# Kernel optimization log

Measured on AMD Instinct MI355X. Metric: run time of the kernel, lower is better.

The kernel has to match this reference:

```python
import jax, jax.numpy as jnp
import numpy as np
import math

# Hardcoded model constants (from source globals)
N_LAYERS = 4
MAX_SEQ_LEN = 34
VOCAB_SIZE = 14
TOK_DIM = 3
POS_DIM = 3
D_MODEL = 6
HEAD_DIM = 3
N_POS = 10
MAX_DIGITS = 10
ANSWER_LEN = 11
X_START, PLUS_POS, Y_START, EQ_POS, Z_START, EOS_POS = 0, 10, 11, 21, 22, 33
PLUS_TOKEN, EQUALS_TOKEN, EOS_TOKEN, PAD_TOKEN = 10, 11, 12, 13
BATCH = 16384


def _spiral(i, p):
    return (math.cos(2 * math.pi * i / p), math.sin(2 * math.pi * i / p), i / max(p - 1, 1))


def _build_pos_enc():
    pe = np.zeros((MAX_SEQ_LEN, POS_DIM), np.float32)
    for i in range(MAX_DIGITS):
        pe[X_START + i] = _spiral(i, N_POS)
    for i in range(MAX_DIGITS):
        pe[Y_START + i] = _spiral(i, N_POS)
    for i in range(min(ANSWER_LEN, N_POS)):
        pe[Z_START + i] = _spiral(i, N_POS)
    pe[Z_START + 10] = [0.0, 0.0, 1.5]
    pe[PLUS_POS] = [2.0, 0.0, -1.0]
    pe[EQ_POS] = [0.0, 2.0, -1.0]
    pe[EOS_POS] = [-2.0, 0.0, -1.0]
    return jnp.asarray(pe)


def _build_tok_emb():
    emb = np.zeros((VOCAB_SIZE, TOK_DIM), np.float32)
    for d in range(10):
        emb[d] = _spiral(d, 10)
    emb[PLUS_TOKEN] = [2.0, 0.0, -1.0]
    emb[EQUALS_TOKEN] = [0.0, 2.0, -1.0]
    emb[EOS_TOKEN] = [-2.0, 0.0, -1.0]
    emb[PAD_TOKEN] = [0.0, -2.0, -1.0]
    return jnp.asarray(emb)


def _xavier(key, shape):
    fan_out, fan_in = shape[-2], shape[-1]
    bound = math.sqrt(6.0 / (fan_in + fan_out))
    return jax.random.uniform(key, shape, jnp.float32, -bound, bound)


def setup_inputs() -> dict:
    key = jax.random.key(0)
    ks = jax.random.split(key, 10)
    L = N_LAYERS
    return {
        "idx": jax.random.randint(ks[0], (BATCH, MAX_SEQ_LEN), 0, VOCAB_SIZE),
        "tok_emb": _build_tok_emb(),
        "pos_enc": _build_pos_enc(),
        "ln_w": jnp.ones((L, D_MODEL), jnp.float32),
        "ln_b": jnp.zeros((L, D_MODEL), jnp.float32),
        "q1w": _xavier(ks[1], (L, HEAD_DIM, TOK_DIM)),
        "k1w": _xavier(ks[2], (L, HEAD_DIM, TOK_DIM)),
        "v1w": _xavier(ks[3], (L, HEAD_DIM, TOK_DIM)),
        "q2w": _xavier(ks[4], (L, HEAD_DIM, POS_DIM)),
        "k2w": _xavier(ks[5], (L, HEAD_DIM, POS_DIM)),
        "v2w": _xavier(ks[6], (L, HEAD_DIM, POS_DIM)),
        "out_w": _xavier(ks[7], (L, D_MODEL, 2 * HEAD_DIM)),
        "lnf_w": jnp.ones((D_MODEL,), jnp.float32),
        "lnf_b": jnp.zeros((D_MODEL,), jnp.float32),
        "head_w": _xavier(ks[8], (VOCAB_SIZE, D_MODEL)),
    }


def _layernorm(x, w, b, eps=1e-5):
    m = jnp.mean(x, -1, keepdims=True)
    v = jnp.mean(jnp.square(x - m), -1, keepdims=True)
    return (x - m) * jax.lax.rsqrt(v + eps) * w + b


def _attend(q, k, v, mask):
    # q,k,v: [B,T,HEAD_DIM]; mask: [T,T] bool lower-triangular
    s = jnp.einsum('bqd,bkd->bqk', q, k) / math.sqrt(HEAD_DIM)
    s = jnp.where(mask, s, jnp.finfo(s.dtype).min)
    return jnp.einsum('bqk,bkd->bqd', jax.nn.softmax(s, axis=-1), v)


def reference(idx, tok_emb, pos_enc, ln_w, ln_b, q1w, k1w, v1w, q2w, k2w, v2w, out_w, lnf_w, lnf_b, head_w):
    B, T = idx.shape
    tok = tok_emb[idx]                                   # [B,T,3]
    pos = jnp.broadcast_to(pos_enc[:T], (B, T, POS_DIM))  # [B,T,3]
    x = jnp.concatenate([tok, pos], axis=-1)             # [B,T,6]
    mask = jnp.tril(jnp.ones((T, T), bool))
    for l in range(N_LAYERS):
        h = _layernorm(x, ln_w[l], ln_b[l])
        ht, hp = h[..., :TOK_DIM], h[..., TOK_DIM:]
        o1 = _attend(ht @ q1w[l].T, ht @ k1w[l].T, ht @ v1w[l].T, mask)
        o2 = _attend(hp @ q2w[l].T, hp @ k2w[l].T, hp @ v2w[l].T, mask)
        x = x + jnp.concatenate([o1, o2], axis=-1) @ out_w[l].T
    x = _layernorm(x, lnf_w, lnf_b)
    return x @ head_w.T                                  # [B,T,VOCAB]
```

## Files before the change

kernel.cpp:

```cpp
#include <hip/hip_runtime.h>
#include <math.h>

#define N_LAYERS 4
#define SEQ      34
#define BATCH_N  16384
#define NE       16
#define NSLOT    8
#define NT       5
#define VOCAB    14
#define QSCALE   0.8329806647638704f

__global__ __launch_bounds__(128) void addtrans_kernel(
    const int*   __restrict__ idx,
    const float* __restrict__ tok_emb,
    const float* __restrict__ pos_enc,
    const float* __restrict__ ln_w,
    const float* __restrict__ ln_b,
    const float* __restrict__ q1w,
    const float* __restrict__ k1w,
    const float* __restrict__ v1w,
    const float* __restrict__ q2w,
    const float* __restrict__ k2w,
    const float* __restrict__ v2w,
    const float* __restrict__ out_w,
    const float* __restrict__ lnf_w,
    const float* __restrict__ lnf_b,
    const float* __restrict__ head_w,
    float* __restrict__ out)
{
    __shared__ float4 kvs[3 * SEQ + 1][NE];

    const int x = threadIdx.x & (NE - 1);
    const int y = threadIdx.x >> 4;
    const int b = (int)blockIdx.x * NE + x;

    int tp[NT];
    tp[0] = (y < 2) ? (32 + y) : (24 + y);
    tp[1] = y;
    tp[2] = 8 + y;
    tp[3] = 16 + y;
    tp[4] = (y < 2) ? (24 + y) : -1;
    const int jmax = tp[0];

    float xs[NT][6];
    #pragma unroll
    for (int k = 0; k < NT; ++k) {
        const int t = tp[k];
        if (t >= 0) {
            const int tok = idx[(size_t)b * SEQ + t];
            xs[k][0] = tok_emb[tok * 3 + 0];
            xs[k][1] = tok_emb[tok * 3 + 1];
            xs[k][2] = tok_emb[tok * 3 + 2];
            xs[k][3] = pos_enc[t * 3 + 0];
            xs[k][4] = pos_enc[t * 3 + 1];
            xs[k][5] = pos_enc[t * 3 + 2];
        }
    }

    float qs[NT][6];

    for (int l = 0; l < N_LAYERS; ++l) {
        __syncthreads();

        #pragma unroll
        for (int k = 0; k < NT; ++k) {
            const int t = tp[k];
            if (t >= 0) {
                float h[6];
                {
                    const float* v = xs[k];
                    float m = (v[0]+v[1]+v[2]+v[3]+v[4]+v[5]) * (1.0f/6.0f);
                    float var = 0.f;
                    #pragma unroll
                    for (int i = 0; i < 6; ++i) { float d = v[i]-m; var += d*d; }
                    var *= (1.0f/6.0f);
                    float r = rsqrtf(var + 1e-5f);
                    #pragma unroll
                    for (int i = 0; i < 6; ++i)
                        h[i] = (v[i]-m) * r * ln_w[l*6+i] + ln_b[l*6+i];
                }
                float kk[6], vv[6];
                #pragma unroll
                for (int i = 0; i < 3; ++i) {
                    const int w = l*9 + i*3;
                    qs[k][i]   = (q1w[w]*h[0] + q1w[w+1]*h[1] + q1w[w+2]*h[2]) * QSCALE;
                    kk[i]      =  k1w[w]*h[0] + k1w[w+1]*h[1] + k1w[w+2]*h[2];
                    vv[i]      =  v1w[w]*h[0] + v1w[w+1]*h[1] + v1w[w+2]*h[2];
                    qs[k][3+i] = (q2w[w]*h[3] + q2w[w+1]*h[4] + q2w[w+2]*h[5]) * QSCALE;
                    kk[3+i]    =  k2w[w]*h[3] + k2w[w+1]*h[4] + k2w[w+2]*h[5];
                    vv[3+i]    =  v2w[w]*h[3] + v2w[w+1]*h[4] + v2w[w+2]*h[5];
                }
                kvs[0*SEQ + t][x] = make_float4(kk[0], kk[1], kk[2], kk[3]);
                kvs[1*SEQ + t][x] = make_float4(kk[4], kk[5], vv[0], vv[1]);
                kvs[2*SEQ + t][x] = make_float4(vv[2], vv[3], vv[4], vv[5]);
            }
        }
        __syncthreads();

        float l1[NT], l2[NT], a[NT][6];
        #pragma unroll
        for (int k = 0; k < NT; ++k) {
            l1[k] = 0.f; l2[k] = 0.f;
            #pragma unroll
            for (int i = 0; i < 6; ++i) a[k][i] = 0.f;
        }
        float4 c0 = kvs[0][x], c1 = kvs[SEQ][x], c2 = kvs[2*SEQ][x];
        #pragma unroll 2
        for (int j = 0; j <= jmax; ++j) {
            float4 n0 = kvs[j + 1][x];
            float4 n1 = kvs[SEQ + j + 1][x];
            float4 n2 = kvs[2*SEQ + j + 1][x];
            #pragma unroll
            for (int k = 0; k < NT; ++k) {
                if (k == 0 || j <= tp[k]) {
                    float s1 = qs[k][0]*c0.x + qs[k][1]*c0.y + qs[k][2]*c0.z;
                    float s2 = qs[k][3]*c0.w + qs[k][4]*c1.x + qs[k][5]*c1.y;
                    float p1 = __builtin_amdgcn_exp2f(s1);
                    float p2 = __builtin_amdgcn_exp2f(s2);
                    l1[k] += p1;        l2[k] += p2;
                    a[k][0] += p1*c1.z; a[k][1] += p1*c1.w; a[k][2] += p1*c2.x;
                    a[k][3] += p2*c2.y; a[k][4] += p2*c2.z; a[k][5] += p2*c2.w;
                }
            }
            c0 = n0; c1 = n1; c2 = n2;
        }

        #pragma unroll
        for (int k = 0; k < NT; ++k) {
            if (tp[k] >= 0) {
                const float i1 = __builtin_amdgcn_rcpf(l1[k]);
                const float i2 = __builtin_amdgcn_rcpf(l2[k]);
                float o[6] = { a[k][0]*i1, a[k][1]*i1, a[k][2]*i1,
                               a[k][3]*i2, a[k][4]*i2, a[k][5]*i2 };
                #pragma unroll
                for (int i = 0; i < 6; ++i) {
                    const int w = l*36 + i*6;
                    xs[k][i] += out_w[w+0]*o[0] + out_w[w+1]*o[1] + out_w[w+2]*o[2]
                              + out_w[w+3]*o[3] + out_w[w+4]*o[4] + out_w[w+5]*o[5];
                }
            }
        }
    }

    #pragma unroll
    for (int k = 0; k < NT; ++k) {
        const int t = tp[k];
        if (t >= 0) {
            float hf[6];
            {
                const float* v = xs[k];
                float m = (v[0]+v[1]+v[2]+v[3]+v[4]+v[5]) * (1.0f/6.0f);
                float var = 0.f;
                #pragma unroll
                for (int i = 0; i < 6; ++i) { float d = v[i]-m; var += d*d; }
                var *= (1.0f/6.0f);
                float r = rsqrtf(var + 1e-5f);
                #pragma unroll
                for (int i = 0; i < 6; ++i)
                    hf[i] = (v[i]-m) * r * lnf_w[i] + lnf_b[i];
            }
            float lg[VOCAB];
            #pragma unroll
            for (int c = 0; c < VOCAB; ++c) {
                const int w = c*6;
                lg[c] = head_w[w+0]*hf[0] + head_w[w+1]*hf[1] + head_w[w+2]*hf[2]
                      + head_w[w+3]*hf[3] + head_w[w+4]*hf[4] + head_w[w+5]*hf[5];
            }
            float2* op = (float2*)(out + ((size_t)b * SEQ + t) * VOCAB);
            #pragma unroll
            for (int c = 0; c < 7; ++c)
                op[c] = make_float2(lg[2*c], lg[2*c+1]);
        }
    }
}

extern "C" void kernel_launch(void* const* d_in, const int* in_sizes, int n_in,
                              void* d_out, int out_size, void* d_ws, size_t ws_size,
                              hipStream_t stream) {
    const int*   idx     = (const int*)  d_in[0];
    const float* tok_emb = (const float*)d_in[1];
    const float* pos_enc = (const float*)d_in[2];
    const float* ln_w    = (const float*)d_in[3];
    const float* ln_b    = (const float*)d_in[4];
    const float* q1w     = (const float*)d_in[5];
    const float* k1w     = (const float*)d_in[6];
    const float* v1w     = (const float*)d_in[7];
    const float* q2w     = (const float*)d_in[8];
    const float* k2w     = (const float*)d_in[9];
    const float* v2w     = (const float*)d_in[10];
    const float* out_w   = (const float*)d_in[11];
    const float* lnf_w   = (const float*)d_in[12];
    const float* lnf_b   = (const float*)d_in[13];
    const float* head_w  = (const float*)d_in[14];
    float* out = (float*)d_out;

    const int grid = BATCH_N / NE;
    addtrans_kernel<<<grid, NE * NSLOT, 0, stream>>>(
        idx, tok_emb, pos_enc, ln_w, ln_b,
        q1w, k1w, v1w, q2w, k2w, v2w,
        out_w, lnf_w, lnf_b, head_w, out);
}
```

Baseline: 146.2 us.

## Restructure causal attention loop into fully unrolled blocks with static row masks

Reassigns rows so each thread holds positions y, 8+y, 16+y, 24+y (plus 32+y for two slots) and rewrites the key loop as a fully unrolled 4x8 block structure. Rows whose keys are entirely in the past are processed unconditionally, and only the diagonal block needs a per-thread mask. This removes the runtime branch per row per key and the software prefetch rotation. It also adds a launch_bounds occupancy hint of 2 blocks. Full unrolling increases code size and may raise register pressure.

```diff
diff --git a/kernel.cpp b/kernel.cpp
--- a/kernel.cpp
+++ b/kernel.cpp
@@ -6,11 +6,22 @@
 #define BATCH_N  16384
 #define NE       16
 #define NSLOT    8
-#define NT       5
+#define NROW     5
 #define VOCAB    14
 #define QSCALE   0.8329806647638704f
 
-__global__ __launch_bounds__(128) void addtrans_kernel(
+#define ATT_BODY(m)                                                        \
+    {                                                                      \
+        float s1 = qs[m][0]*c0.x + qs[m][1]*c0.y + qs[m][2]*c0.z;          \
+        float s2 = qs[m][3]*c0.w + qs[m][4]*c1.x + qs[m][5]*c1.y;          \
+        float p1 = __builtin_amdgcn_exp2f(s1);                             \
+        float p2 = __builtin_amdgcn_exp2f(s2);                             \
+        l1[m] += p1;          l2[m] += p2;                                 \
+        a[m][0] += p1*c1.z;   a[m][1] += p1*c1.w;   a[m][2] += p1*c2.x;    \
+        a[m][3] += p2*c2.y;   a[m][4] += p2*c2.z;   a[m][5] += p2*c2.w;    \
+    }
+
+__global__ __launch_bounds__(128, 2) void addtrans_kernel(
     const int*   __restrict__ idx,
     const float* __restrict__ tok_emb,
     const float* __restrict__ pos_enc,
@@ -34,17 +45,16 @@
     const int y = threadIdx.x >> 4;
     const int b = (int)blockIdx.x * NE + x;
 
-    int tp[NT];
-    tp[0] = (y < 2) ? (32 + y) : (24 + y);
-    tp[1] = y;
-    tp[2] = 8 + y;
-    tp[3] = 16 + y;
-    tp[4] = (y < 2) ? (24 + y) : -1;
-    const int jmax = tp[0];
-
-    float xs[NT][6];
+    int tp[NROW];
+    tp[0] = y;
+    tp[1] = 8 + y;
+    tp[2] = 16 + y;
+    tp[3] = 24 + y;
+    tp[4] = (y < 2) ? (32 + y) : -1;
+
+    float xs[NROW][6];
     #pragma unroll
-    for (int k = 0; k < NT; ++k) {
+    for (int k = 0; k < NROW; ++k) {
         const int t = tp[k];
         if (t >= 0) {
             const int tok = idx[(size_t)b * SEQ + t];
@@ -57,13 +67,13 @@
         }
     }
 
-    float qs[NT][6];
+    float qs[NROW][6];
 
     for (int l = 0; l < N_LAYERS; ++l) {
         __syncthreads();
 
         #pragma unroll
-        for (int k = 0; k < NT; ++k) {
+        for (int k = 0; k < NROW; ++k) {
             const int t = tp[k];
             if (t >= 0) {
                 float h[6];
@@ -97,53 +107,55 @@
         }
         __syncthreads();
 
-        float l1[NT], l2[NT], a[NT][6];
-        #pragma unroll
-        for (int k = 0; k < NT; ++k) {
+        float l1[NROW], l2[NROW], a[NROW][6];
+        #pragma unroll
+        for (int k = 0; k < NROW; ++k) {
             l1[k] = 0.f; l2[k] = 0.f;
             #pragma unroll
             for (int i = 0; i < 6; ++i) a[k][i] = 0.f;
         }
-        float4 c0 = kvs[0][x], c1 = kvs[SEQ][x], c2 = kvs[2*SEQ][x];
-        #pragma unroll 2
-        for (int j = 0; j <= jmax; ++j) {
-            float4 n0 = kvs[j + 1][x];
-            float4 n1 = kvs[SEQ + j + 1][x];
-            float4 n2 = kvs[2*SEQ + j + 1][x];
-            #pragma unroll
-            for (int k = 0; k < NT; ++k) {
-                if (k == 0 || j <= tp[k]) {
-                    float s1 = qs[k][0]*c0.x + qs[k][1]*c0.y + qs[k][2]*c0.z;
-                    float s2 = qs[k][3]*c0.w + qs[k][4]*c1.x + qs[k][5]*c1.y;
-                    float p1 = __builtin_amdgcn_exp2f(s1);
-                    float p2 = __builtin_amdgcn_exp2f(s2);
-                    l1[k] += p1;        l2[k] += p2;
-                    a[k][0] += p1*c1.z; a[k][1] += p1*c1.w; a[k][2] += p1*c2.x;
-                    a[k][3] += p2*c2.y; a[k][4] += p2*c2.z; a[k][5] += p2*c2.w;
-                }
-            }
-            c0 = n0; c1 = n1; c2 = n2;
-        }
-
-        #pragma unroll
-        for (int k = 0; k < NT; ++k) {
+
+        #pragma unroll
+        for (int o = 0; o < 4; ++o) {
+            #pragma unroll
+            for (int jp = 0; jp < 8; ++jp) {
+                const int j = 8 * o + jp;
+                float4 c0 = kvs[j][x];
+                float4 c1 = kvs[SEQ + j][x];
+                float4 c2 = kvs[2*SEQ + j][x];
+                #pragma unroll
+                for (int m = o + 1; m < 4; ++m) ATT_BODY(m);
+                if (jp <= y)     ATT_BODY(o);
+                if (j <= tp[4])  ATT_BODY(4);
+            }
+        }
+        #pragma unroll
+        for (int j = 32; j < 34; ++j) {
+            float4 c0 = kvs[j][x];
+            float4 c1 = kvs[SEQ + j][x];
+            float4 c2 = kvs[2*SEQ + j][x];
+            if (j <= tp[4]) ATT_BODY(4);
+        }
+
+        #pragma unroll
+        for (int k = 0; k < NROW; ++k) {
             if (tp[k] >= 0) {
                 const float i1 = __builtin_amdgcn_rcpf(l1[k]);
                 const float i2 = __builtin_amdgcn_rcpf(l2[k]);
-                float o[6] = { a[k][0]*i1, a[k][1]*i1, a[k][2]*i1,
-                               a[k][3]*i2, a[k][4]*i2, a[k][5]*i2 };
+                float o6[6] = { a[k][0]*i1, a[k][1]*i1, a[k][2]*i1,
+                                a[k][3]*i2, a[k][4]*i2, a[k][5]*i2 };
                 #pragma unroll
                 for (int i = 0; i < 6; ++i) {
                     const int w = l*36 + i*6;
-                    xs[k][i] += out_w[w+0]*o[0] + out_w[w+1]*o[1] + out_w[w+2]*o[2]
-                              + out_w[w+3]*o[3] + out_w[w+4]*o[4] + out_w[w+5]*o[5];
+                    xs[k][i] += out_w[w+0]*o6[0] + out_w[w+1]*o6[1] + out_w[w+2]*o6[2]
+                              + out_w[w+3]*o6[3] + out_w[w+4]*o6[4] + out_w[w+5]*o6[5];
                 }
             }
         }
     }
 
     #pragma unroll
-    for (int k = 0; k < NT; ++k) {
+    for (int k = 0; k < NROW; ++k) {
         const int t = tp[k];
         if (t >= 0) {
             float hf[6];
```

New measurement: 215.3 us. +47.3%, slower.
